# Performance work log

Measured on AMD Instinct MI355X. Metric: run time of the kernel, lower is better.

## Reference

```python
import jax, jax.numpy as jnp
from jax import lax
import numpy as np

NUM_CLASS = 80
N_PROP = 256
C_FEAT, H_FEAT, W_FEAT = 1024, 50, 80
IMG_H, IMG_W = 800, 1280
POOL = 14
SPATIAL_SCALE = 0.0625
SCORE_THR = 0.5
NMS_THR = 0.7
K_PRE = 1000   # pre-NMS candidate cap (jit-static stand-in for boolean filter)
K_OUT = 200    # keep[:200] in source
BW = (10.0, 10.0, 5.0, 5.0)
SCALE_CLAMP = float(np.log(1000.0 / 16.0))


def setup_inputs() -> dict:
    key = jax.random.key(0)
    ks = jax.random.split(key, 9)
    features = jax.random.normal(ks[0], (1, C_FEAT, H_FEAT, W_FEAT), jnp.float32)
    x1 = jax.random.uniform(ks[1], (N_PROP,), minval=0.0, maxval=IMG_W - 64.0)
    y1 = jax.random.uniform(ks[2], (N_PROP,), minval=0.0, maxval=IMG_H - 64.0)
    w = jax.random.uniform(ks[3], (N_PROP,), minval=32.0, maxval=320.0)
    h = jax.random.uniform(ks[4], (N_PROP,), minval=32.0, maxval=320.0)
    proposals = jnp.stack([x1, y1, jnp.minimum(x1 + w, float(IMG_W)),
                           jnp.minimum(y1 + h, float(IMG_H))], axis=1)
    d_in = C_FEAT * POOL * POOL
    w_fc = jax.random.normal(ks[5], (d_in, 1024), jnp.float32) / np.sqrt(d_in)
    b_fc = jnp.zeros((1024,), jnp.float32)
    # scale class head up so softmax produces confident (>0.5) detections
    w_cls = jax.random.normal(ks[6], (1024, NUM_CLASS + 1), jnp.float32) * (8.0 / np.sqrt(1024))
    b_cls = jnp.zeros((NUM_CLASS + 1,), jnp.float32)
    w_box = jax.random.normal(ks[7], (1024, NUM_CLASS * 4), jnp.float32) / np.sqrt(1024)
    b_box = jnp.zeros((NUM_CLASS * 4,), jnp.float32)
    return {"features": features, "proposals": proposals, "w_fc": w_fc, "b_fc": b_fc,
            "w_cls": w_cls, "b_cls": b_cls, "w_box": w_box, "b_box": b_box}


def roi_align(features, rois):
    """torchvision RoIAlign (aligned=False), output 14x14, one sample per bin.
    features: [1,C,H,W], rois: [N,4] xyxy. Returns [N,C,14,14]."""
    f = features[0]                               # [C,H,W]
    H, W = f.shape[1], f.shape[2]
    x1 = rois[:, 0] * SPATIAL_SCALE
    y1 = rois[:, 1] * SPATIAL_SCALE
    x2 = rois[:, 2] * SPATIAL_SCALE
    y2 = rois[:, 3] * SPATIAL_SCALE
    rw = jnp.maximum(x2 - x1, 1.0)
    rh = jnp.maximum(y2 - y1, 1.0)
    bw = rw / POOL
    bh = rh / POOL
    grid = jnp.arange(POOL, dtype=jnp.float32) + 0.5
    xs = x1[:, None] + grid[None, :] * bw[:, None]      # [N,P] bin-center x
    ys = y1[:, None] + grid[None, :] * bh[:, None]      # [N,P] bin-center y
    Y = jnp.broadcast_to(ys[:, :, None], (rois.shape[0], POOL, POOL))
    X = jnp.broadcast_to(xs[:, None, :], (rois.shape[0], POOL, POOL))
    valid = (Y >= -1.0) & (Y <= H) & (X >= -1.0) & (X <= W)
    y = jnp.clip(Y, 0.0, H - 1.0)
    x = jnp.clip(X, 0.0, W - 1.0)
    y0 = jnp.floor(y).astype(jnp.int32)
    x0 = jnp.floor(x).astype(jnp.int32)
    y1i = jnp.minimum(y0 + 1, H - 1)
    x1i = jnp.minimum(x0 + 1, W - 1)
    ly = y - y0; lx = x - x0; hy = 1.0 - ly; hx = 1.0 - lx
    g = lambda yi, xi: f[:, yi, xi]               # -> [C,N,P,P]
    val = ((hy * hx) * g(y0, x0) + (hy * lx) * g(y0, x1i)
           + (ly * hx) * g(y1i, x0) + (ly * lx) * g(y1i, x1i))
    val = val * valid.astype(val.dtype)
    return jnp.transpose(val, (1, 0, 2, 3))       # [N,C,P,P]


def apply_deltas(boxes, deltas):
    """boxes,deltas: [..., 4]; detectron-style delta apply with weights BW."""
    w = boxes[..., 2] - boxes[..., 0]
    h = boxes[..., 3] - boxes[..., 1]
    cx = boxes[..., 0] + 0.5 * w
    cy = boxes[..., 1] + 0.5 * h
    dx = deltas[..., 0] / BW[0]
    dy = deltas[..., 1] / BW[1]
    dw = jnp.minimum(deltas[..., 2] / BW[2], SCALE_CLAMP)
    dh = jnp.minimum(deltas[..., 3] / BW[3], SCALE_CLAMP)
    pcx = dx * w + cx
    pcy = dy * h + cy
    pw = jnp.exp(dw) * w
    ph = jnp.exp(dh) * h
    return jnp.stack([pcx - 0.5 * pw, pcy - 0.5 * ph,
                      pcx + 0.5 * pw, pcy + 0.5 * ph], axis=-1)


def _iou_matrix(b):
    area = jnp.maximum(b[:, 2] - b[:, 0], 0.0) * jnp.maximum(b[:, 3] - b[:, 1], 0.0)
    lt = jnp.maximum(b[:, None, :2], b[None, :, :2])
    rb = jnp.minimum(b[:, None, 2:], b[None, :, 2:])
    wh = jnp.clip(rb - lt, 0.0)
    inter = wh[..., 0] * wh[..., 1]
    return inter / jnp.maximum(area[:, None] + area[None, :] - inter, 1e-9)


def forward(features, proposals, w_fc, b_fc, w_cls, b_cls, w_box, b_box):
    feat = roi_align(features, proposals)                 # [N,1024,14,14]
    x = feat.reshape(feat.shape[0], -1) @ w_fc + b_fc     # [N,1024]
    logits = x @ w_cls + b_cls                            # [N,81]
    deltas = x @ w_box + b_box                            # [N,320]
    scores = jax.nn.softmax(logits, axis=-1)[:, 1:]       # [N,80] drop bg

    # per-class box-delta apply (proposal expanded over classes)
    boxes = apply_deltas(jnp.broadcast_to(proposals[:, None, :], (N_PROP, NUM_CLASS, 4)),
                         deltas.reshape(N_PROP, NUM_CLASS, 4))
    boxes = jnp.stack([jnp.clip(boxes[..., 0], 0.0, float(IMG_W)),
                       jnp.clip(boxes[..., 1], 0.0, float(IMG_H)),
                       jnp.clip(boxes[..., 2], 0.0, float(IMG_W)),
                       jnp.clip(boxes[..., 3], 0.0, float(IMG_H))], axis=-1)

    # flatten (proposal, class) candidates; mask = score > 0.5 (boolean filter in source)
    s_flat = scores.reshape(-1)
    b_flat = boxes.reshape(-1, 4)
    c_flat = jnp.broadcast_to(jnp.arange(NUM_CLASS)[None, :], (N_PROP, NUM_CLASS)).reshape(-1)
    masked = jnp.where(s_flat > SCORE_THR, s_flat, -1.0)
    top_s, top_i = lax.top_k(masked, K_PRE)              # score-sorted candidates
    cand_b = b_flat[top_i]
    cand_c = c_flat[top_i]
    cand_valid = top_s > SCORE_THR

    # batched NMS: offset boxes by class so classes never interact
    off = cand_c.astype(jnp.float32) * float(IMG_W + 1)
    iou = _iou_matrix(cand_b + off[:, None])
    idxs = jnp.arange(K_PRE)

    def body(keep, xs):
        i, row = xs
        kept_i = keep[i]
        suppress = kept_i & (row > NMS_THR) & (idxs > i)
        return keep & ~suppress, kept_i

    _, kept = lax.scan(body, cand_valid, (idxs, iou))

    # compact kept candidates (already score-ordered) into top-200 slots
    rank = jnp.cumsum(kept.astype(jnp.int32)) - 1
    slot = jnp.where(kept, rank, K_OUT)  # out-of-range -> dropped
    out_boxes = jnp.zeros((K_OUT, 4), cand_b.dtype).at[slot].set(cand_b, mode='drop')
    out_scores = jnp.zeros((K_OUT,), top_s.dtype).at[slot].set(top_s, mode='drop')
    out_classes = jnp.full((K_OUT,), -1, jnp.int32).at[slot].set(cand_c.astype(jnp.int32), mode='drop')
    return out_boxes, out_scores, out_classes


def reference(features, proposals, w_fc, b_fc, w_cls, b_cls, w_box, b_box):
    return forward(features, proposals, w_fc, b_fc, w_cls, b_cls, w_box, b_box)
```

## Files before the change

### kernel.cpp

```cpp
#include <hip/hip_runtime.h>
#include <math.h>

#define N_PROP 256
#define NUM_CLASS 80
#define H_FEAT 50
#define W_FEAT 80
#define K_DIM 200704
#define D_HID 1024
#define SPATIAL_SCALE 0.0625f
#define SCALE_CLAMP 4.135166556742356f
#define IMG_W_F 1280.0f
#define IMG_H_F 800.0f

typedef unsigned short ushort_t;
typedef __attribute__((ext_vector_type(8))) short short8v;
typedef __attribute__((ext_vector_type(16))) float f32x16;
typedef __attribute__((ext_vector_type(4))) float f32x4v;
typedef __attribute__((ext_vector_type(4))) unsigned short ushort4v;
typedef __attribute__((ext_vector_type(2))) unsigned short ushort2v;

__device__ __forceinline__ unsigned short f2bf(float f) {
  unsigned int u = __builtin_bit_cast(unsigned int, f);
  u += 0x7FFFu + ((u >> 16) & 1u);
  return (unsigned short)(u >> 16);
}
__device__ __forceinline__ float bf2f(unsigned short h) {
  unsigned int u = ((unsigned int)h) << 16;
  return __builtin_bit_cast(float, u);
}

__global__ void roi_kernel(const float* __restrict__ F, const float* __restrict__ props,
                           ushort_t* __restrict__ Ahi, ushort_t* __restrict__ Alo) {
  const int tid = threadIdx.x;
  const int m = blockIdx.y;
  const int cg = blockIdx.x;
  __shared__ float w00[196], w01[196], w10[196], w11[196];
  __shared__ int o00[196], o01[196], o10[196], o11[196];
  const float x1s = props[m*4+0]*SPATIAL_SCALE;
  const float y1s = props[m*4+1]*SPATIAL_SCALE;
  const float x2s = props[m*4+2]*SPATIAL_SCALE;
  const float y2s = props[m*4+3]*SPATIAL_SCALE;
  const float bwf = fmaxf(x2s-x1s, 1.0f) / 14.0f;
  const float bhf = fmaxf(y2s-y1s, 1.0f) / 14.0f;
  if (tid < 196) {
    int ph = tid / 14, pw = tid - ph*14;
    float X = x1s + (pw + 0.5f)*bwf;
    float Y = y1s + (ph + 0.5f)*bhf;
    bool valid = (Y >= -1.0f) && (Y <= (float)H_FEAT) && (X >= -1.0f) && (X <= (float)W_FEAT);
    float x = fminf(fmaxf(X, 0.0f), (float)(W_FEAT-1));
    float y = fminf(fmaxf(Y, 0.0f), (float)(H_FEAT-1));
    float xf = floorf(x), yf = floorf(y);
    int ix0 = (int)xf, iy0 = (int)yf;
    int ix1 = min(ix0+1, W_FEAT-1), iy1 = min(iy0+1, H_FEAT-1);
    float lx = x-xf, ly = y-yf, hx = 1.0f-lx, hy = 1.0f-ly;
    float v = valid ? 1.0f : 0.0f;
    w00[tid] = hy*hx*v; w01[tid] = hy*lx*v; w10[tid] = ly*hx*v; w11[tid] = ly*lx*v;
    o00[tid] = iy0*W_FEAT+ix0; o01[tid] = iy0*W_FEAT+ix1;
    o10[tid] = iy1*W_FEAT+ix0; o11[tid] = iy1*W_FEAT+ix1;
  }
  __syncthreads();
  const int base_c = cg*128;
  const size_t rowbase = (size_t)m*K_DIM + (size_t)base_c*196;
  for (int it = 0; it < 49; ++it) {
    int i2 = it*512 + tid*2;
    int c = i2 / 196;
    int b = i2 - c*196;
    const float* f = F + (size_t)(base_c + c)*4000;
    float v0 = w00[b]*f[o00[b]] + w01[b]*f[o01[b]] + w10[b]*f[o10[b]] + w11[b]*f[o11[b]];
    float v1 = w00[b+1]*f[o00[b+1]] + w01[b+1]*f[o01[b+1]] + w10[b+1]*f[o10[b+1]] + w11[b+1]*f[o11[b+1]];
    unsigned short h0 = f2bf(v0), h1 = f2bf(v1);
    ushort2v hv; hv[0] = h0; hv[1] = h1;
    ushort2v lv; lv[0] = f2bf(v0 - bf2f(h0)); lv[1] = f2bf(v1 - bf2f(h1));
    *(ushort2v*)&Ahi[rowbase + i2] = hv;
    *(ushort2v*)&Alo[rowbase + i2] = lv;
  }
}

__global__ __launch_bounds__(512, 2) void mfma_gemm(
    const ushort_t* __restrict__ Ahi, const ushort_t* __restrict__ Alo,
    const float* __restrict__ B, float* __restrict__ P, int steps_per, int nwg) {
  __shared__ ushort_t lds[32768];
  const int tid = threadIdx.x;
  const int wv = tid >> 6, lane = tid & 63, l31 = lane & 31, lhi = lane >> 5;
  const int wm = wv >> 2, wn = wv & 3;
  int id = blockIdx.x;
  int nid = ((nwg & 7) == 0) ? ((id & 7) * (nwg >> 3) + (id >> 3)) : id;
  const int bn = (nid & 3) * 256;
  const int z  = nid >> 2;
  const int step0 = z * steps_per;
  int steps = steps_per;
  if (step0 + steps > 6272) steps = 6272 - step0;

  f32x16 acc[4][2];
  #pragma unroll
  for (int a = 0; a < 4; ++a)
    #pragma unroll
    for (int b = 0; b < 2; ++b)
      #pragma unroll
      for (int e = 0; e < 16; ++e) acc[a][b][e] = 0.0f;

  if (steps > 0) {
    const int H = steps * 2;
    const ushort_t* asrc[2];
    #pragma unroll
    for (int i = 0; i < 2; ++i) {
      int s = i*512 + tid;
      int plane = s >> 9, kb = (s >> 8) & 1, row = s & 255;
      const ushort_t* basep = plane ? Alo : Ahi;
      asrc[i] = basep + (size_t)row * K_DIM + step0*32 + kb*8;
    }
    const int p = tid >> 6, c4 = tid & 63;
    const bool bstage = (tid < 256);
    const float* bsrc = B + (size_t)(step0*32 + 4*p) * D_HID + bn + c4*4;
    const unsigned bkbh = (unsigned)(p >> 1) * 2048u, bsub = (unsigned)((p & 1) * 4);

    #define STAGE_A(bufn) do { \
      _Pragma("unroll") \
      for (int i = 0; i < 2; ++i) { \
        __builtin_amdgcn_global_load_lds(asrc[i], &lds[(bufn) + (i*512 + tid - lane + lane)*8], 16, 0, 0); \
        asrc[i] += 16; } \
    } while (0)

    #define LOAD_B() do { \
      if (bstage) { \
        b0 = __builtin_nontemporal_load((const f32x4v*)(bsrc)); \
        b1 = __builtin_nontemporal_load((const f32x4v*)(bsrc + D_HID)); \
        b2 = __builtin_nontemporal_load((const f32x4v*)(bsrc + 2*D_HID)); \
        b3 = __builtin_nontemporal_load((const f32x4v*)(bsrc + 3*D_HID)); \
      } \
      bsrc += 16 * D_HID; \
    } while (0)

    #define WRITE_B(bufn) do { \
      if (bstage) { \
        _Pragma("unroll") \
        for (int cc = 0; cc < 4; ++cc) { \
          float g0 = b0[cc], g1 = b1[cc], g2 = b2[cc], g3 = b3[cc]; \
          ushort4v hv, lv; \
          hv[0]=f2bf(g0); lv[0]=f2bf(g0-bf2f(hv[0])); \
          hv[1]=f2bf(g1); lv[1]=f2bf(g1-bf2f(hv[1])); \
          hv[2]=f2bf(g2); lv[2]=f2bf(g2-bf2f(hv[2])); \
          hv[3]=f2bf(g3); lv[3]=f2bf(g3-bf2f(hv[3])); \
          int col = c4*4 + cc, scol = col ^ ((col>>3)&7); \
          unsigned idx = (bufn) + 8192u + bkbh + (unsigned)scol*8u + bsub; \
          *(ushort4v*)&lds[idx] = hv; \
          *(ushort4v*)&lds[idx + 4096] = lv; \
        } \
      } \
    } while (0)

    #define COMPUTE(bufn) do { \
      short8v ah[4], al[4], bh[2], bl[2]; \
      _Pragma("unroll") \
      for (int ms = 0; ms < 4; ++ms) { \
        unsigned ai = (bufn) + (unsigned)(lhi*2048 + (wm*128 + ms*32 + l31)*8); \
        ah[ms] = *(const short8v*)&lds[ai]; \
        al[ms] = *(const short8v*)&lds[ai + 4096]; \
      } \
      _Pragma("unroll") \
      for (int ns = 0; ns < 2; ++ns) { \
        int col = wn*64 + ns*32 + l31, scol = col ^ ((col>>3)&7); \
        unsigned bi = (bufn) + 8192u + (unsigned)(lhi*2048 + scol*8); \
        bh[ns] = *(const short8v*)&lds[bi]; \
        bl[ns] = *(const short8v*)&lds[bi + 4096]; \
      } \
      _Pragma("unroll") \
      for (int ms = 0; ms < 4; ++ms) \
        _Pragma("unroll") \
        for (int ns = 0; ns < 2; ++ns) { \
          acc[ms][ns] = __builtin_amdgcn_mfma_f32_32x32x16_bf16(ah[ms], bh[ns], acc[ms][ns], 0, 0, 0); \
          acc[ms][ns] = __builtin_amdgcn_mfma_f32_32x32x16_bf16(ah[ms], bl[ns], acc[ms][ns], 0, 0, 0); \
          acc[ms][ns] = __builtin_amdgcn_mfma_f32_32x32x16_bf16(al[ms], bh[ns], acc[ms][ns], 0, 0, 0); \
        } \
    } while (0)

    f32x4v b0, b1, b2, b3;
    STAGE_A(0u);
    LOAD_B();
    WRITE_B(0u);
    __syncthreads();
    unsigned cur = 0;
    for (int h = 0; h < H; ++h) {
      const bool last = (h == H - 1);
      if (!last) {
        STAGE_A(cur ^ 16384u);
        LOAD_B();
      }
      COMPUTE(cur);
      if (!last) WRITE_B(cur ^ 16384u);
      __syncthreads();
      cur ^= 16384u;
    }
    #undef STAGE_A
    #undef LOAD_B
    #undef WRITE_B
    #undef COMPUTE
  }
  float* Pp = P + (size_t)z * (N_PROP * D_HID);
  #pragma unroll
  for (int ms = 0; ms < 4; ++ms)
    #pragma unroll
    for (int ns = 0; ns < 2; ++ns)
      #pragma unroll
      for (int r = 0; r < 16; ++r) {
        int row = wm*128 + ms*32 + (r & 3) + 8*(r >> 2) + 4*lhi;
        int col = bn + wn*64 + ns*32 + l31;
        __builtin_nontemporal_store(acc[ms][ns][r], &Pp[(size_t)row * D_HID + col]);
      }
}

__global__ void reduce_kernel(const float* __restrict__ P, float* __restrict__ X, int ksplit) {
  int i = blockIdx.x*256 + threadIdx.x;
  f32x4v s = {0.0f, 0.0f, 0.0f, 0.0f};
  const f32x4v* P4 = (const f32x4v*)P;
  for (int r = 0; r < ksplit; ++r) s += P4[(size_t)r*65536 + i];
  ((f32x4v*)X)[i] = s;
}

__global__ void heads_kernel(const float* __restrict__ X, const float* __restrict__ bfc,
                             const float* __restrict__ wcls, const float* __restrict__ bcls,
                             const float* __restrict__ wbox, const float* __restrict__ bbox,
                             float* __restrict__ scores, float* __restrict__ deltas,
                             float* __restrict__ keym) {
  const int tid = threadIdx.x, m = blockIdx.x;
  __shared__ float xs[1024];
  __shared__ float lg[81];
  __shared__ float red[2];
  #pragma unroll
  for (int r = 0; r < 4; ++r) {
    int k = r*256 + tid;
    xs[k] = X[m*1024 + k] + bfc[k];
  }
  __syncthreads();
  for (int j = tid; j < 401; j += 256) {
    if (j < 81) {
      const float* w = wcls + j;
      float accv = bcls[j];
      #pragma unroll 8
      for (int k = 0; k < 1024; ++k) accv = fmaf(xs[k], w[(size_t)k*81], accv);
      lg[j] = accv;
    } else {
      int jb = j - 81;
      const float* w = wbox + jb;
      float accv = bbox[jb];
      #pragma unroll 8
      for (int k = 0; k < 1024; ++k) accv = fmaf(xs[k], w[(size_t)k*320], accv);
      deltas[m*320 + jb] = accv;
    }
  }
  __syncthreads();
  if (tid == 0) {
    float mx = lg[0]; int amax = 0;
    for (int j = 1; j < 81; ++j) if (lg[j] > mx) { mx = lg[j]; amax = j; }
    float sm = 0.0f;
    for (int j = 0; j < 81; ++j) sm += expf(lg[j]-mx);
    float m2 = -1e30f;
    for (int j = 0; j < 81; ++j) if (j != amax) m2 = fmaxf(m2, lg[j]);
    float s2 = 0.0f;
    for (int j = 0; j < 81; ++j) if (j != amax) s2 += expf(lg[j]-m2);
    keym[m] = (m2 - mx) + logf(s2);
    red[0] = mx; red[1] = sm;
  }
  __syncthreads();
  if (tid < 80) scores[m*80 + tid] = expf(lg[tid+1]-red[0]) / red[1];
}

__global__ void detect_kernel(const float* __restrict__ scores, const float* __restrict__ deltas,
                              const float* __restrict__ props, const float* __restrict__ keym,
                              float* __restrict__ out) {
  const int tid = threadIdx.x;
  __shared__ int s_cnt;
  __shared__ float g_key[256];
  __shared__ float g_score[256];
  __shared__ int   g_idx[256];
  __shared__ float c_score[256];
  __shared__ int   c_idx[256];
  __shared__ float bxs[256][4];
  __shared__ int   bcls[256];
  __shared__ unsigned long long supp[256][4];
  if (tid == 0) s_cnt = 0;
  g_key[tid] = 1e30f; g_score[tid] = -1.0f; g_idx[tid] = 0x7FFFFFFF;
  c_score[tid] = -1.0f; c_idx[tid] = 0x7FFFFFFF;
  bxs[tid][0] = bxs[tid][1] = bxs[tid][2] = bxs[tid][3] = 0.0f;
  bcls[tid] = 0;
  __syncthreads();
  for (int t = 0; t < 80; ++t) {
    int i = t*256 + tid;
    float s = scores[i];
    if (s > 0.5f) {
      int p = atomicAdd(&s_cnt, 1);
      if (p < 256) { g_score[p] = s; g_idx[p] = i; g_key[p] = keym[i/80]; }
    }
  }
  __syncthreads();
  const int C = min(s_cnt, 256);
  if (tid < C) {
    float kt = g_key[tid]; int si = g_idx[tid]; float st = g_score[tid];
    int rank = 0;
    for (int u = 0; u < C; ++u) {
      float ku = g_key[u]; int iu = g_idx[u];
      if ((ku < kt) || (ku == kt && iu < si)) ++rank;
    }
    c_score[rank] = st; c_idx[rank] = si;
  }
  __syncthreads();
  if (tid < C) {
    int fi = c_idx[tid];
    int m = fi / 80, j = fi - m*80;
    float px1 = props[m*4+0], py1 = props[m*4+1], px2 = props[m*4+2], py2 = props[m*4+3];
    float w = px2-px1, h = py2-py1;
    float cx = px1 + 0.5f*w, cy = py1 + 0.5f*h;
    const float* d = deltas + m*320 + j*4;
    float dx = d[0]/10.0f, dy = d[1]/10.0f;
    float dw = fminf(d[2]/5.0f, SCALE_CLAMP), dh = fminf(d[3]/5.0f, SCALE_CLAMP);
    float pcx = dx*w + cx, pcy = dy*h + cy;
    float pw = expf(dw)*w, ph = expf(dh)*h;
    bxs[tid][0] = fminf(fmaxf(pcx - 0.5f*pw, 0.0f), IMG_W_F);
    bxs[tid][1] = fminf(fmaxf(pcy - 0.5f*ph, 0.0f), IMG_H_F);
    bxs[tid][2] = fminf(fmaxf(pcx + 0.5f*pw, 0.0f), IMG_W_F);
    bxs[tid][3] = fminf(fmaxf(pcy + 0.5f*ph, 0.0f), IMG_H_F);
    bcls[tid] = j;
  }
  __syncthreads();
  unsigned long long row[4] = {0,0,0,0};
  if (tid < C) {
    float ax1=bxs[tid][0], ay1=bxs[tid][1], ax2=bxs[tid][2], ay2=bxs[tid][3];
    float aarea = fmaxf(ax2-ax1,0.f)*fmaxf(ay2-ay1,0.f);
    int acl = bcls[tid];
    for (int j2 = tid+1; j2 < C; ++j2) {
      if (bcls[j2] != acl) continue;
      float b1=bxs[j2][0], b2=bxs[j2][1], b3=bxs[j2][2], b4=bxs[j2][3];
      float barea = fmaxf(b3-b1,0.f)*fmaxf(b4-b2,0.f);
      float iw = fmaxf(fminf(ax2,b3) - fmaxf(ax1,b1), 0.f);
      float ih = fmaxf(fminf(ay2,b4) - fmaxf(ay1,b2), 0.f);
      float inter = iw*ih;
      float iou = inter / fmaxf(aarea + barea - inter, 1e-9f);
      if (iou > 0.7f) row[j2>>6] |= (1ull << (j2 & 63));
    }
  }
  supp[tid][0]=row[0]; supp[tid][1]=row[1]; supp[tid][2]=row[2]; supp[tid][3]=row[3];
  __syncthreads();
  for (int i = tid; i < 1200; i += 256) out[i] = (i >= 1000) ? -1.0f : 0.0f;
  __syncthreads();
  if (tid == 0) {
    unsigned long long rem[4] = {0,0,0,0};
    int oc = 0;
    for (int i = 0; i < C; ++i) {
      if ((rem[i>>6] >> (i & 63)) & 1ull) continue;
      if (oc < 200) {
        out[oc*4+0]=bxs[i][0]; out[oc*4+1]=bxs[i][1]; out[oc*4+2]=bxs[i][2]; out[oc*4+3]=bxs[i][3];
        out[800+oc]  = c_score[i];
        out[1000+oc] = (float)bcls[i];
      }
      ++oc;
      rem[0]|=supp[i][0]; rem[1]|=supp[i][1]; rem[2]|=supp[i][2]; rem[3]|=supp[i][3];
    }
  }
}

extern "C" void kernel_launch(void* const* d_in, const int* in_sizes, int n_in,
                              void* d_out, int out_size, void* d_ws, size_t ws_size,
                              hipStream_t stream) {
  const float* F     = (const float*)d_in[0];
  const float* props = (const float*)d_in[1];
  const float* wfc   = (const float*)d_in[2];
  const float* bfc   = (const float*)d_in[3];
  const float* wcls  = (const float*)d_in[4];
  const float* bcls  = (const float*)d_in[5];
  const float* wbox  = (const float*)d_in[6];
  const float* bbox  = (const float*)d_in[7];
  float* out = (float*)d_out;
  char* wsb  = (char*)d_ws;

  const size_t abytes = (size_t)N_PROP * K_DIM * 2;
  ushort_t* Ahi = (ushort_t*)wsb;
  ushort_t* Alo = (ushort_t*)(wsb + abytes);
  float* X  = (float*)(wsb + 2*abytes);
  float* SC = X + 262144;
  float* DL = SC + 20480;
  float* KM = DL + 81920;
  float* P  = KM + 256;
  const size_t fixed = 2*abytes + (size_t)(262144 + 20480 + 81920 + 256) * 4;
  if (ws_size < fixed + 2u*1048576u) {
    (void)hipMemsetAsync(d_out, 0x7F, (size_t)out_size*sizeof(float), stream);
    return;
  }
  int ksplit = (int)((ws_size - fixed) / ((size_t)N_PROP * D_HID * 4));
  if (ksplit > 64) ksplit = 64;
  if (ksplit >= 8) ksplit &= ~7;
  const int steps_per = (6272 + ksplit - 1) / ksplit;
  const int nwg = 4 * ksplit;

  roi_kernel   <<<dim3(8, N_PROP),    256, 0, stream>>>(F, props, Ahi, Alo);
  mfma_gemm    <<<nwg,                512, 0, stream>>>(Ahi, Alo, wfc, P, steps_per, nwg);
  reduce_kernel<<<256,                256, 0, stream>>>(P, X, ksplit);
  heads_kernel <<<N_PROP,             256, 0, stream>>>(X, bfc, wcls, bcls, wbox, bbox, SC, DL, KM);
  detect_kernel<<<1,                  256, 0, stream>>>(SC, DL, props, KM, out);
}
```

Measured before the change: 803.8 us.

## Triple-buffer A tiles in LDS with manual waitcnt pipelining and MFMA priority

The GEMM's LDS use is split into three A buffers and two B buffers, so A tiles are prefetched two steps ahead through global_load_lds while B stays double-buffered. The blanket __syncthreads is replaced with explicit vmcnt/lgkmcnt waits, s_barrier and sched_barrier, so outstanding A loads can stay in flight across iterations. s_setprio is raised around the MFMA block to favour compute waves. The larger LDS footprint may limit occupancy, and the hand-counted waitcnt values must match the issued loads exactly.

```diff
diff --git a/kernel.cpp b/kernel.cpp
--- a/kernel.cpp
+++ b/kernel.cpp
@@ -79,7 +79,7 @@
 __global__ __launch_bounds__(512, 2) void mfma_gemm(
     const ushort_t* __restrict__ Ahi, const ushort_t* __restrict__ Alo,
     const float* __restrict__ B, float* __restrict__ P, int steps_per, int nwg) {
-  __shared__ ushort_t lds[32768];
+  __shared__ ushort_t lds[40960];
   const int tid = threadIdx.x;
   const int wv = tid >> 6, lane = tid & 63, l31 = lane & 31, lhi = lane >> 5;
   const int wm = wv >> 2, wn = wv & 3;
@@ -114,10 +114,10 @@
     const float* bsrc = B + (size_t)(step0*32 + 4*p) * D_HID + bn + c4*4;
     const unsigned bkbh = (unsigned)(p >> 1) * 2048u, bsub = (unsigned)((p & 1) * 4);
 
-    #define STAGE_A(bufn) do { \
+    #define STAGE_A(aoff) do { \
       _Pragma("unroll") \
       for (int i = 0; i < 2; ++i) { \
-        __builtin_amdgcn_global_load_lds(asrc[i], &lds[(bufn) + (i*512 + tid - lane + lane)*8], 16, 0, 0); \
+        __builtin_amdgcn_global_load_lds(asrc[i], &lds[(aoff) + (unsigned)(i*512 + tid)*8u], 16, 0, 0); \
         asrc[i] += 16; } \
     } while (0)
 
@@ -131,7 +131,7 @@
       bsrc += 16 * D_HID; \
     } while (0)
 
-    #define WRITE_B(bufn) do { \
+    #define WRITE_B(boff) do { \
       if (bstage) { \
         _Pragma("unroll") \
         for (int cc = 0; cc < 4; ++cc) { \
@@ -142,28 +142,29 @@
           hv[2]=f2bf(g2); lv[2]=f2bf(g2-bf2f(hv[2])); \
           hv[3]=f2bf(g3); lv[3]=f2bf(g3-bf2f(hv[3])); \
           int col = c4*4 + cc, scol = col ^ ((col>>3)&7); \
-          unsigned idx = (bufn) + 8192u + bkbh + (unsigned)scol*8u + bsub; \
+          unsigned idx = (boff) + bkbh + (unsigned)scol*8u + bsub; \
           *(ushort4v*)&lds[idx] = hv; \
           *(ushort4v*)&lds[idx + 4096] = lv; \
         } \
       } \
     } while (0)
 
-    #define COMPUTE(bufn) do { \
+    #define COMPUTE(aoff, boff) do { \
       short8v ah[4], al[4], bh[2], bl[2]; \
       _Pragma("unroll") \
       for (int ms = 0; ms < 4; ++ms) { \
-        unsigned ai = (bufn) + (unsigned)(lhi*2048 + (wm*128 + ms*32 + l31)*8); \
+        unsigned ai = (aoff) + (unsigned)(lhi*2048 + (wm*128 + ms*32 + l31)*8); \
         ah[ms] = *(const short8v*)&lds[ai]; \
         al[ms] = *(const short8v*)&lds[ai + 4096]; \
       } \
       _Pragma("unroll") \
       for (int ns = 0; ns < 2; ++ns) { \
         int col = wn*64 + ns*32 + l31, scol = col ^ ((col>>3)&7); \
-        unsigned bi = (bufn) + 8192u + (unsigned)(lhi*2048 + scol*8); \
+        unsigned bi = (boff) + (unsigned)(lhi*2048 + scol*8); \
         bh[ns] = *(const short8v*)&lds[bi]; \
         bl[ns] = *(const short8v*)&lds[bi + 4096]; \
       } \
+      __builtin_amdgcn_s_setprio(1); \
       _Pragma("unroll") \
       for (int ms = 0; ms < 4; ++ms) \
         _Pragma("unroll") \
@@ -172,24 +173,37 @@
           acc[ms][ns] = __builtin_amdgcn_mfma_f32_32x32x16_bf16(ah[ms], bl[ns], acc[ms][ns], 0, 0, 0); \
           acc[ms][ns] = __builtin_amdgcn_mfma_f32_32x32x16_bf16(al[ms], bh[ns], acc[ms][ns], 0, 0, 0); \
         } \
+      __builtin_amdgcn_s_setprio(0); \
     } while (0)
 
     f32x4v b0, b1, b2, b3;
+    LOAD_B();
     STAGE_A(0u);
-    LOAD_B();
-    WRITE_B(0u);
-    __syncthreads();
-    unsigned cur = 0;
+    STAGE_A(8192u);
+    asm volatile("s_waitcnt vmcnt(4)" ::: "memory");
+    __builtin_amdgcn_sched_barrier(0);
+    WRITE_B(24576u);
+    asm volatile("s_waitcnt vmcnt(2)" ::: "memory");
+    asm volatile("s_waitcnt lgkmcnt(0)" ::: "memory");
+    __builtin_amdgcn_s_barrier();
+    __builtin_amdgcn_sched_barrier(0);
+
+    unsigned aC = 0u, aN = 8192u, aNN = 16384u;
+    unsigned bC = 24576u, bN = 32768u;
     for (int h = 0; h < H; ++h) {
-      const bool last = (h == H - 1);
-      if (!last) {
-        STAGE_A(cur ^ 16384u);
-        LOAD_B();
-      }
-      COMPUTE(cur);
-      if (!last) WRITE_B(cur ^ 16384u);
-      __syncthreads();
-      cur ^= 16384u;
+      const int rem = H - 1 - h;
+      if (rem > 0) LOAD_B();
+      if (rem > 1) STAGE_A(aNN);
+      COMPUTE(aC, bC);
+      if (rem > 1)       asm volatile("s_waitcnt vmcnt(2)" ::: "memory");
+      else if (rem == 1) asm volatile("s_waitcnt vmcnt(0)" ::: "memory");
+      __builtin_amdgcn_sched_barrier(0);
+      if (rem > 0) WRITE_B(bN);
+      asm volatile("s_waitcnt lgkmcnt(0)" ::: "memory");
+      __builtin_amdgcn_s_barrier();
+      __builtin_amdgcn_sched_barrier(0);
+      unsigned t = aC; aC = aN; aN = aNN; aNN = t;
+      t = bC; bC = bN; bN = t;
     }
     #undef STAGE_A
     #undef LOAD_B
```

After: 798.4 us, median of 2. Within noise of the previous version (-0.7%).

## Stage B via direct-to-LDS loads in 4-deep pipeline, convert bf16 split at compute

Applied to the files above, without the earlier changes.

Replaces the register-staged fp32 B load and bf16 hi/lo conversion with global_load_lds of raw fp32 B tiles into LDS. The single double-buffered LDS ring becomes a 4-stage ring of 128KB, kept three tiles ahead and ordered with explicit vmcnt waits plus one barrier per step. The bf16 hi/lo split of B now happens per wave at compute time, and MFMA issue priority is raised with s_setprio. This aims to hide global-load latency and remove the VGPR round trip and second barrier. In exchange, every wave redoes the B conversion, B is read from LDS with scalar unswizzled loads, and the larger LDS footprint may cut occupancy below the 2 blocks per CU the launch bounds request.

```diff
diff --git a/kernel.cpp b/kernel.cpp
--- a/kernel.cpp
+++ b/kernel.cpp
@@ -16,7 +16,6 @@
 typedef __attribute__((ext_vector_type(8))) short short8v;
 typedef __attribute__((ext_vector_type(16))) float f32x16;
 typedef __attribute__((ext_vector_type(4))) float f32x4v;
-typedef __attribute__((ext_vector_type(4))) unsigned short ushort4v;
 typedef __attribute__((ext_vector_type(2))) unsigned short ushort2v;
 
 __device__ __forceinline__ unsigned short f2bf(float f) {
@@ -79,7 +78,7 @@
 __global__ __launch_bounds__(512, 2) void mfma_gemm(
     const ushort_t* __restrict__ Ahi, const ushort_t* __restrict__ Alo,
     const float* __restrict__ B, float* __restrict__ P, int steps_per, int nwg) {
-  __shared__ ushort_t lds[32768];
+  __shared__ __align__(16) unsigned char smem[131072];
   const int tid = threadIdx.x;
   const int wv = tid >> 6, lane = tid & 63, l31 = lane & 31, lhi = lane >> 5;
   const int wm = wv >> 2, wn = wv & 3;
@@ -109,61 +108,50 @@
       const ushort_t* basep = plane ? Alo : Ahi;
       asrc[i] = basep + (size_t)row * K_DIM + step0*32 + kb*8;
     }
-    const int p = tid >> 6, c4 = tid & 63;
-    const bool bstage = (tid < 256);
-    const float* bsrc = B + (size_t)(step0*32 + 4*p) * D_HID + bn + c4*4;
-    const unsigned bkbh = (unsigned)(p >> 1) * 2048u, bsub = (unsigned)((p & 1) * 4);
-
-    #define STAGE_A(bufn) do { \
+    const float* bsrc[2];
+    #pragma unroll
+    for (int i = 0; i < 2; ++i) {
+      int s = i*512 + tid;
+      int krow = s >> 6, col4 = s & 63;
+      bsrc[i] = B + (size_t)(step0*32 + krow) * D_HID + bn + col4*4;
+    }
+
+    #define ISSUE(h) do { \
+      unsigned ab_ = (unsigned)((h) & 3) * 16384u; \
+      unsigned bb_ = 65536u + (unsigned)((h) & 3) * 16384u; \
       _Pragma("unroll") \
       for (int i = 0; i < 2; ++i) { \
-        __builtin_amdgcn_global_load_lds(asrc[i], &lds[(bufn) + (i*512 + tid - lane + lane)*8], 16, 0, 0); \
+        __builtin_amdgcn_global_load_lds(asrc[i], &smem[ab_ + (unsigned)(i*512 + tid)*16u], 16, 0, 0); \
         asrc[i] += 16; } \
+      _Pragma("unroll") \
+      for (int i = 0; i < 2; ++i) { \
+        __builtin_amdgcn_global_load_lds(bsrc[i], &smem[bb_ + (unsigned)(i*512 + tid)*16u], 16, 0, 0); \
+        bsrc[i] += 16 * D_HID; } \
     } while (0)
 
-    #define LOAD_B() do { \
-      if (bstage) { \
-        b0 = __builtin_nontemporal_load((const f32x4v*)(bsrc)); \
-        b1 = __builtin_nontemporal_load((const f32x4v*)(bsrc + D_HID)); \
-        b2 = __builtin_nontemporal_load((const f32x4v*)(bsrc + 2*D_HID)); \
-        b3 = __builtin_nontemporal_load((const f32x4v*)(bsrc + 3*D_HID)); \
+    #define COMPUTE(h) do { \
+      unsigned ab_ = (unsigned)((h) & 3) * 16384u; \
+      unsigned bb_ = 65536u + (unsigned)((h) & 3) * 16384u; \
+      short8v ah[4], al[4], bh[2], bl[2]; \
+      _Pragma("unroll") \
+      for (int ms = 0; ms < 4; ++ms) { \
+        unsigned abyte = ab_ + (unsigned)(lhi*4096 + (wm*128 + ms*32 + l31)*16); \
+        ah[ms] = *(const short8v*)&smem[abyte]; \
+        al[ms] = *(const short8v*)&smem[abyte + 8192u]; \
       } \
-      bsrc += 16 * D_HID; \
-    } while (0)
-
-    #define WRITE_B(bufn) do { \
-      if (bstage) { \
+      _Pragma("unroll") \
+      for (int ns = 0; ns < 2; ++ns) { \
+        int col = wn*64 + ns*32 + l31; \
+        unsigned bbyte = bb_ + (unsigned)lhi*8192u + (unsigned)col*4u; \
         _Pragma("unroll") \
-        for (int cc = 0; cc < 4; ++cc) { \
-          float g0 = b0[cc], g1 = b1[cc], g2 = b2[cc], g3 = b3[cc]; \
-          ushort4v hv, lv; \
-          hv[0]=f2bf(g0); lv[0]=f2bf(g0-bf2f(hv[0])); \
-          hv[1]=f2bf(g1); lv[1]=f2bf(g1-bf2f(hv[1])); \
-          hv[2]=f2bf(g2); lv[2]=f2bf(g2-bf2f(hv[2])); \
-          hv[3]=f2bf(g3); lv[3]=f2bf(g3-bf2f(hv[3])); \
-          int col = c4*4 + cc, scol = col ^ ((col>>3)&7); \
-          unsigned idx = (bufn) + 8192u + bkbh + (unsigned)scol*8u + bsub; \
-          *(ushort4v*)&lds[idx] = hv; \
-          *(ushort4v*)&lds[idx + 4096] = lv; \
+        for (int j = 0; j < 8; ++j) { \
+          float g = *(const float*)&smem[bbyte + (unsigned)j*1024u]; \
+          unsigned short h16 = f2bf(g); \
+          bh[ns][j] = (short)h16; \
+          bl[ns][j] = (short)f2bf(g - bf2f(h16)); \
         } \
       } \
-    } while (0)
-
-    #define COMPUTE(bufn) do { \
-      short8v ah[4], al[4], bh[2], bl[2]; \
-      _Pragma("unroll") \
-      for (int ms = 0; ms < 4; ++ms) { \
-        unsigned ai = (bufn) + (unsigned)(lhi*2048 + (wm*128 + ms*32 + l31)*8); \
-        ah[ms] = *(const short8v*)&lds[ai]; \
-        al[ms] = *(const short8v*)&lds[ai + 4096]; \
-      } \
-      _Pragma("unroll") \
-      for (int ns = 0; ns < 2; ++ns) { \
-        int col = wn*64 + ns*32 + l31, scol = col ^ ((col>>3)&7); \
-        unsigned bi = (bufn) + 8192u + (unsigned)(lhi*2048 + scol*8); \
-        bh[ns] = *(const short8v*)&lds[bi]; \
-        bl[ns] = *(const short8v*)&lds[bi + 4096]; \
-      } \
+      __builtin_amdgcn_s_setprio(1); \
       _Pragma("unroll") \
       for (int ms = 0; ms < 4; ++ms) \
         _Pragma("unroll") \
@@ -172,28 +160,23 @@
           acc[ms][ns] = __builtin_amdgcn_mfma_f32_32x32x16_bf16(ah[ms], bl[ns], acc[ms][ns], 0, 0, 0); \
           acc[ms][ns] = __builtin_amdgcn_mfma_f32_32x32x16_bf16(al[ms], bh[ns], acc[ms][ns], 0, 0, 0); \
         } \
+      __builtin_amdgcn_s_setprio(0); \
     } while (0)
 
-    f32x4v b0, b1, b2, b3;
-    STAGE_A(0u);
-    LOAD_B();
-    WRITE_B(0u);
-    __syncthreads();
-    unsigned cur = 0;
+    const int pre = (H < 3) ? H : 3;
+    for (int hp = 0; hp < pre; ++hp) ISSUE(hp);
     for (int h = 0; h < H; ++h) {
-      const bool last = (h == H - 1);
-      if (!last) {
-        STAGE_A(cur ^ 16384u);
-        LOAD_B();
-      }
-      COMPUTE(cur);
-      if (!last) WRITE_B(cur ^ 16384u);
-      __syncthreads();
-      cur ^= 16384u;
-    }
-    #undef STAGE_A
-    #undef LOAD_B
-    #undef WRITE_B
+      const int rem = H - 1 - h;
+      if (rem >= 2)      asm volatile("s_waitcnt vmcnt(8)" ::: "memory");
+      else if (rem == 1) asm volatile("s_waitcnt vmcnt(4)" ::: "memory");
+      else               asm volatile("s_waitcnt vmcnt(0)" ::: "memory");
+      __builtin_amdgcn_sched_barrier(0);
+      __builtin_amdgcn_s_barrier();
+      __builtin_amdgcn_sched_barrier(0);
+      if (h + 3 < H) ISSUE(h + 3);
+      COMPUTE(h);
+    }
+    #undef ISSUE
     #undef COMPUTE
   }
   float* Pp = P + (size_t)z * (N_PROP * D_HID);
```

New measurement: 839.0 us. 4.4% more time.
